# Performance work log

Hardware: AMD Instinct MI355X
Metric: run time of the kernel (lower is better)

## Reference

```python
import jax, jax.numpy as jnp
import numpy as np

THRESH = 0.5
MARGIN = 0.1
SCALE_POS = 2.0
SCALE_NEG = 50.0
EPS = 1e-5


def setup_inputs() -> dict:
    key = jax.random.key(0)
    k1, k2 = jax.random.split(key)
    B, D = 8192, 256
    feats = jax.random.normal(k1, (B, D), dtype=jnp.float32)
    # speaker embeddings are L2-normalized (cosine similarity, thresh=0.5 assumes this)
    feats = feats / jnp.linalg.norm(feats, axis=-1, keepdims=True)
    labels = jax.random.randint(k2, (B,), 0, 512, dtype=jnp.int64)
    return {"feats": feats, "labels": labels}


def reference(feats, labels):
    B = feats.shape[0]
    sim = jnp.matmul(feats, feats.T)                      # [B, B]
    same = labels[:, None] == labels[None, :]             # [B, B]

    pos_mask = same & (sim < 1.0 - EPS)                   # pos_pair_ (drops self-sim ~1)
    neg_mask = ~same                                      # neg_pair_

    neg_inf = jnp.float32(-jnp.inf)
    pos_inf = jnp.float32(jnp.inf)
    min_pos = jnp.min(jnp.where(pos_mask, sim, pos_inf), axis=1)  # min(pos_pair_)
    max_neg = jnp.max(jnp.where(neg_mask, sim, neg_inf), axis=1)  # max(neg_pair_)

    # dynamic re-masking (hard mining)
    neg_sel = neg_mask & (sim > (min_pos - MARGIN)[:, None])
    pos_sel = pos_mask & (sim < (max_neg + MARGIN)[:, None])

    valid = jnp.any(neg_sel, axis=1) & jnp.any(pos_sel, axis=1)

    # masked sums of exponentials via exp(-inf)=0; single fused mask+exp+sum
    pos_sum = jnp.sum(jnp.exp(jnp.where(pos_sel, -SCALE_POS * (sim - THRESH), neg_inf)), axis=1)
    neg_sum = jnp.sum(jnp.exp(jnp.where(neg_sel, SCALE_NEG * (sim - THRESH), neg_inf)), axis=1)

    row_loss = (1.0 / SCALE_POS) * jnp.log1p(pos_sum) + (1.0 / SCALE_NEG) * jnp.log1p(neg_sum)
    loss = jnp.sum(jnp.where(valid, row_loss, 0.0)) / B
    prec1 = jnp.mean(1.0 - valid.astype(jnp.float32))
    return loss, prec1
```

## Files before the change

kernel.cpp:

```cpp
#include <hip/hip_runtime.h>
#include <stdint.h>


typedef __attribute__((ext_vector_type(8))) short short8;
typedef __attribute__((ext_vector_type(4))) float floatx4;

constexpr int D = 256;
constexpr int BM = 128;
constexpr int NT = 64;
constexpr int NPB = NT * 8;
constexpr int BT = 512;
constexpr int CHUNK_SH = BM * 64;
constexpr int RECCAP = 2048;

__device__ __forceinline__ unsigned f2bf(float f) {
  unsigned u = __float_as_uint(f);
  return (u + 0x7FFFu + ((u >> 16) & 1u)) >> 16;
}

__device__ __forceinline__ void gl_lds16(const void* g, void* l) {
  __builtin_amdgcn_global_load_lds(
      (const __attribute__((address_space(1))) unsigned int*)g,
      (__attribute__((address_space(3))) unsigned int*)l, 16, 0, 0);
}

__device__ __forceinline__ unsigned fkey(float f) {
  unsigned b = __float_as_uint(f);
  return (b & 0x80000000u) ? ~b : (b | 0x80000000u);
}
__device__ __forceinline__ float fdec(unsigned k) {
  unsigned b = (k & 0x80000000u) ? (k & 0x7FFFFFFFu) : ~k;
  return __uint_as_float(b);
}

__device__ __forceinline__ void pair1_body(
    int bid, const unsigned short* __restrict__ fb, const int* __restrict__ labels,
    unsigned* __restrict__ kmin, unsigned* __restrict__ kmax,
    uint2* __restrict__ recs, int* __restrict__ reccnt,
    short* As, short* Bs, int* labA, int* emitCnt) {
  const int I   = bid >> 3;
  const int g   = bid & 7;
  const int nT  = (I < 32) ? 33 : 32;
  const int t0  = (g * nT) >> 3;
  const int t1  = ((g + 1) * nT) >> 3;
  const int row0 = I * BM;

  const int tid  = threadIdx.x;
  const int lane = tid & 63;
  const int wave = tid >> 6;
  const int l15  = lane & 15;
  const int quad = lane >> 4;
  const int wr   = (wave >> 1) * 32;
  const int wc   = (wave & 1) * 64;

  const float ONE_EPS = 1.0f - 1e-5f;
  const float INF = __builtin_inff();

  if (tid == 0) *emitCnt = 0;
  __syncthreads();
  if (tid < BM) labA[tid] = labels[row0 + tid];

  auto stage = [&](int b, int col0, int kc) {
#pragma unroll
    for (int j = 0; j < 2; ++j) {
      int idx = j * BT + tid;
      int r   = idx >> 3;
      int sl  = idx & 7;
      int cb  = sl ^ (r & 7);
      const char* ga = (const char*)fb + (((size_t)(row0 + r)) << 9) + (kc << 7) + (cb << 4);
      const char* gb = (const char*)fb + (((size_t)(col0 + r)) << 9) + (kc << 7) + (cb << 4);
      gl_lds16(ga, (char*)As + (size_t)b * (CHUNK_SH * 2) + ((size_t)idx << 4));
      gl_lds16(gb, (char*)Bs + (size_t)b * (CHUNK_SH * 2) + ((size_t)idx << 4));
    }
  };

  int arow[2], brow[4];
#pragma unroll
  for (int i = 0; i < 2; ++i) arow[i] = wr + i * 16 + l15;
#pragma unroll
  for (int i = 0; i < 4; ++i) brow[i] = wc + i * 16 + l15;

  float s0[8], s1[8];
#pragma unroll
  for (int i = 0; i < 8; ++i) { s0[i] = INF; s1[i] = -INF; }

  stage(0, ((I + t0) & 63) * BM, 0);

  int cur = 0;
  for (int off = t0; off < t1; ++off) {
    const int J = (I + off) & 63;
    const int col0 = J * BM;
    const bool diag = (off == 0);

    int labc[4], cidx[4];
#pragma unroll
    for (int cf = 0; cf < 4; ++cf) {
      int ci = col0 + wc + cf * 16 + l15;
      cidx[cf] = ci;
      labc[cf] = labels[ci];
    }

    floatx4 acc[2][4];
#pragma unroll
    for (int rf = 0; rf < 2; ++rf)
#pragma unroll
      for (int cf = 0; cf < 4; ++cf)
        acc[rf][cf] = (floatx4)(0.f);

#pragma unroll
    for (int kc = 0; kc < 4; ++kc) {
      if (kc < 3) {
        stage(cur ^ 1, col0, kc + 1);
        asm volatile("s_waitcnt vmcnt(4)" ::: "memory");
      } else if (off + 1 < t1) {
        stage(cur ^ 1, ((I + off + 1) & 63) * BM, 0);
        asm volatile("s_waitcnt vmcnt(4)" ::: "memory");
      } else {
        asm volatile("s_waitcnt vmcnt(0)" ::: "memory");
      }
      __builtin_amdgcn_s_barrier();
      asm volatile("" ::: "memory");

      const short* Ab = As + cur * CHUNK_SH;
      const short* Bb = Bs + cur * CHUNK_SH;
#pragma unroll
      for (int ks = 0; ks < 2; ++ks) {
        const int gg = ks * 4 + quad;
        short8 a[2], b[4];
#pragma unroll
        for (int rf = 0; rf < 2; ++rf)
          a[rf] = *(const short8*)(Ab + arow[rf] * 64 + ((gg ^ (arow[rf] & 7)) << 3));
#pragma unroll
        for (int cf = 0; cf < 4; ++cf)
          b[cf] = *(const short8*)(Bb + brow[cf] * 64 + ((gg ^ (brow[cf] & 7)) << 3));
#pragma unroll
        for (int rf = 0; rf < 2; ++rf)
#pragma unroll
          for (int cf = 0; cf < 4; ++cf)
            acc[rf][cf] = __builtin_amdgcn_mfma_f32_16x16x32_bf16(a[rf], b[cf], acc[rf][cf], 0, 0, 0);
      }
      asm volatile("s_waitcnt lgkmcnt(0)" ::: "memory");
      __builtin_amdgcn_s_barrier();
      asm volatile("" ::: "memory");
      cur ^= 1;
    }

    float c0[4], c1[4];
#pragma unroll
    for (int i = 0; i < 4; ++i) { c0[i] = INF; c1[i] = -INF; }

#pragma unroll
    for (int rf = 0; rf < 2; ++rf) {
#pragma unroll
      for (int r = 0; r < 4; ++r) {
        const int ri = wr + rf * 16 + quad * 4 + r;
        const int lr = labA[ri];
#pragma unroll
        for (int cf = 0; cf < 4; ++cf) {
          float sim = acc[rf][cf][r];
          bool same = (lr == labc[cf]);
          bool posok = same && (sim < ONE_EPS);
          float pc = posok ? sim : INF;
          float nc = same ? -INF : sim;
          s0[rf * 4 + r] = fminf(s0[rf * 4 + r], pc);
          s1[rf * 4 + r] = fmaxf(s1[rf * 4 + r], nc);
          c0[cf] = fminf(c0[cf], pc);
          c1[cf] = fmaxf(c1[cf], nc);
          bool hotn = (!same) && (sim > 0.22f);
          if (posok || hotn) {
            unsigned key = (unsigned)(row0 + ri) | ((unsigned)cidx[cf] << 13) |
                           (diag ? (1u << 26) : 0u) | (hotn ? (1u << 27) : 0u);
            int slot = atomicAdd(emitCnt, 1);
            if (slot < RECCAP)
              recs[(size_t)bid * RECCAP + slot] = make_uint2(key, __float_as_uint(sim));
          }
        }
      }
    }

    if (!diag) {
#pragma unroll
      for (int cf = 0; cf < 4; ++cf) {
        float v = c0[cf], w = c1[cf];
#pragma unroll
        for (int m = 16; m < 64; m <<= 1) {
          float vv = __shfl_xor(v, m), ww = __shfl_xor(w, m);
          v = fminf(v, vv);
          w = fmaxf(w, ww);
        }
        if (quad == 0) {
          atomicMin(&kmin[cidx[cf]], fkey(v));
          atomicMax(&kmax[cidx[cf]], fkey(w));
        }
      }
    }
  }

#pragma unroll
  for (int i = 0; i < 8; ++i) {
#pragma unroll
    for (int m = 1; m < 16; m <<= 1) {
      float v = __shfl_xor(s0[i], m), w = __shfl_xor(s1[i], m);
      s0[i] = fminf(s0[i], v);
      s1[i] = fmaxf(s1[i], w);
    }
  }
  if (l15 == 0) {
#pragma unroll
    for (int rf = 0; rf < 2; ++rf)
#pragma unroll
      for (int r = 0; r < 4; ++r) {
        int ri = row0 + wr + rf * 16 + quad * 4 + r;
        atomicMin(&kmin[ri], fkey(s0[rf * 4 + r]));
        atomicMax(&kmax[ri], fkey(s1[rf * 4 + r]));
      }
  }
  __syncthreads();
  if (tid == 0) reccnt[bid] = (*emitCnt < RECCAP) ? *emitCnt : RECCAP;
}

__device__ __forceinline__ void apply_body(
    int bid, const uint2* __restrict__ recs, const int* __restrict__ reccnt,
    const float* __restrict__ tmn, const float* __restrict__ tmx,
    float* __restrict__ pos_acc, float* __restrict__ neg_acc) {
  const int cnt = reccnt[bid];
  for (int k = threadIdx.x; k < cnt; k += blockDim.x) {
    uint2 rec = recs[(size_t)bid * RECCAP + k];
    int ri = rec.x & 8191;
    int ci = (rec.x >> 13) & 8191;
    bool dg = (rec.x >> 26) & 1;
    bool ng = (rec.x >> 27) & 1;
    float sim = __uint_as_float(rec.y);
    if (!ng) {
      float e = __expf(fmaf(-2.f, sim, 1.f));
      if (sim < tmx[ri])        atomicAdd(&pos_acc[ri], e);
      if (!dg && sim < tmx[ci]) atomicAdd(&pos_acc[ci], e);
    } else {
      float e = __expf(fmaf(50.f, sim, -25.f));
      if (sim > tmn[ri])        atomicAdd(&neg_acc[ri], e);
      if (!dg && sim > tmn[ci]) atomicAdd(&neg_acc[ci], e);
    }
  }
}

__device__ __forceinline__ void final_body(
    int T, const int* __restrict__ labels, const int* __restrict__ labcnt,
    const float* __restrict__ pos_acc, const float* __restrict__ neg_acc,
    const float* __restrict__ tmn, const float* __restrict__ tmx,
    const float* __restrict__ mpv, const float* __restrict__ mnv,
    float* __restrict__ out, float* sred) {
  const int tid = threadIdx.x;
  float loss = 0.f, cval = 0.f;
  if (tid < 128) {
    int r = T * 128 + tid;
    float a = pos_acc[r];
    float b = neg_acc[r] + (float)(8192 - labcnt[labels[r]]) * 1e-30f;
    bool valid = (mnv[r] > tmn[r]) && (mpv[r] < tmx[r]);
    if (valid) {
      loss = 0.5f * log1pf(a) + 0.02f * log1pf(b);
      cval = 1.f;
    }
  }
#pragma unroll
  for (int m = 1; m < 64; m <<= 1) {
    loss += __shfl_xor(loss, m);
    cval += __shfl_xor(cval, m);
  }
  int wv = tid >> 6, ln = tid & 63;
  if (ln == 0) { sred[wv] = loss; sred[8 + wv] = cval; }
  __syncthreads();
  if (tid == 0) {
    float L = 0.f, C = 0.f;
#pragma unroll
    for (int w = 0; w < 8; ++w) { L += sred[w]; C += sred[8 + w]; }
    atomicAdd(out, L / 8192.0f);
    atomicAdd(out + 1, -C / 8192.0f);
  }
}

__global__ void k_convert(const float* __restrict__ feats, unsigned short* __restrict__ fb,
                          float* __restrict__ pos_acc, float* __restrict__ neg_acc,
                          unsigned* __restrict__ kmin, unsigned* __restrict__ kmax,
                          int* __restrict__ labcnt, float* __restrict__ out, int n4) {
  int i = blockIdx.x * blockDim.x + threadIdx.x;
  if (i < n4) {
    float4 v = ((const float4*)feats)[i];
    unsigned lo = f2bf(v.x) | (f2bf(v.y) << 16);
    unsigned hi = f2bf(v.z) | (f2bf(v.w) << 16);
    ((uint2*)fb)[i] = make_uint2(lo, hi);
  }
  if (i < 8192) {
    pos_acc[i] = 0.f;
    neg_acc[i] = 0.f;
    kmin[i] = 0xFFFFFFFFu;
    kmax[i] = 0u;
  }
  if (i < 512) labcnt[i] = 0;
  if (i == 0) { out[0] = 0.f; out[1] = 1.f; }
}

__global__ __launch_bounds__(BT, 4)
void k_pair1(const unsigned short* __restrict__ fb, const int* __restrict__ labels,
             unsigned* __restrict__ kmin, unsigned* __restrict__ kmax,
             uint2* __restrict__ recs, int* __restrict__ reccnt) {
  __shared__ __align__(16) short As[2 * CHUNK_SH];
  __shared__ __align__(16) short Bs[2 * CHUNK_SH];
  __shared__ int labA[BM];
  __shared__ int emitCnt;
  pair1_body(blockIdx.x, fb, labels, kmin, kmax, recs, reccnt,
             As, Bs, labA, &emitCnt);
}

__global__ void k_thresh(const unsigned* __restrict__ kmin, const unsigned* __restrict__ kmax,
                         const int* __restrict__ labels, int* __restrict__ labcnt,
                         float* __restrict__ tmn, float* __restrict__ tmx,
                         float* __restrict__ mpv, float* __restrict__ mnv) {
  int r = blockIdx.x * blockDim.x + threadIdx.x;
  if (r < 8192) {
    float a = fdec(kmin[r]);
    float b = fdec(kmax[r]);
    tmn[r] = a - 0.1f;
    tmx[r] = b + 0.1f;
    mpv[r] = a;
    mnv[r] = b;
    atomicAdd(&labcnt[labels[r]], 1);
  }
}

__global__ void k_apply(const uint2* __restrict__ recs, const int* __restrict__ reccnt,
                        const float* __restrict__ tmn, const float* __restrict__ tmx,
                        float* __restrict__ pos_acc, float* __restrict__ neg_acc) {
  apply_body(blockIdx.x, recs, reccnt, tmn, tmx, pos_acc, neg_acc);
}

__global__ __launch_bounds__(BT)
void k_final(const int* __restrict__ labels, const int* __restrict__ labcnt,
             const float* __restrict__ pos_acc, const float* __restrict__ neg_acc,
             const float* __restrict__ tmn, const float* __restrict__ tmx,
             const float* __restrict__ mpv, const float* __restrict__ mnv,
             float* __restrict__ out) {
  __shared__ float sred[16];
  final_body(blockIdx.x, labels, labcnt, pos_acc, neg_acc, tmn, tmx, mpv, mnv,
             out, sred);
}

extern "C" void kernel_launch(void* const* d_in, const int* in_sizes, int n_in,
                              void* d_out, int out_size, void* d_ws, size_t ws_size,
                              hipStream_t stream) {
  const float* feats  = (const float*)d_in[0];
  const int*   labels = (const int*)d_in[1];
  const int Bn = in_sizes[1];
  float* out = (float*)d_out;

  char* base = (char*)d_ws;
  unsigned short* fb = (unsigned short*)base;
  size_t o = (size_t)Bn * D * 2;
  uint2* recs = (uint2*)(base + o); o += (size_t)NPB * RECCAP * 8;
  unsigned* kmin = (unsigned*)(base + o); o += (size_t)Bn * 4;
  unsigned* kmax = (unsigned*)(base + o); o += (size_t)Bn * 4;
  float* tmn = (float*)(base + o);  o += (size_t)Bn * 4;
  float* tmx = (float*)(base + o);  o += (size_t)Bn * 4;
  float* mpv = (float*)(base + o);  o += (size_t)Bn * 4;
  float* mnv = (float*)(base + o);  o += (size_t)Bn * 4;
  float* pos_acc = (float*)(base + o); o += (size_t)Bn * 4;
  float* neg_acc = (float*)(base + o); o += (size_t)Bn * 4;
  int* labcnt = (int*)(base + o);   o += 512 * 4;
  int* reccnt = (int*)(base + o);   o += (size_t)NPB * 4;

  int n4 = Bn * D / 4;
  k_convert<<<(n4 + 255) / 256, 256, 0, stream>>>(feats, fb, pos_acc, neg_acc,
                                                  kmin, kmax, labcnt, out, n4);
  k_pair1<<<NPB, BT, 0, stream>>>(fb, labels, kmin, kmax, recs, reccnt);
  k_thresh<<<64, 128, 0, stream>>>(kmin, kmax, labels, labcnt, tmn, tmx, mpv, mnv);
  k_apply<<<NPB, 256, 0, stream>>>(recs, reccnt, tmn, tmx, pos_acc, neg_acc);
  k_final<<<NT, BT, 0, stream>>>(labels, labcnt, pos_acc, neg_acc,
                                 tmn, tmx, mpv, mnv, out);
}
```

Measured before the change: 120.2 us.

## Keep full A row-block in LDS, stream B from global, drop thresh kernel

The pair kernel now loads the block's 128 rows × 256 bf16 A tile into LDS once and reads B fragments directly from global memory (L2) instead of double-buffering both A and B chunks through LDS with barriers. Block IDs are swizzled across XCDs so blocks sharing a row-block land on the same XCD for L2 reuse. The k_thresh kernel is removed: label counting moves into the pair kernel, and apply/final decode kmin/kmax inline. This removes a launch and the per-chunk barriers, but uncoalesced direct global B loads without prefetch may expose latency.

```diff
diff --git a/kernel.cpp b/kernel.cpp
--- a/kernel.cpp
+++ b/kernel.cpp
@@ -10,7 +10,7 @@
 constexpr int NT = 64;
 constexpr int NPB = NT * 8;
 constexpr int BT = 512;
-constexpr int CHUNK_SH = BM * 64;
+constexpr int ASH = BM * D;
 constexpr int RECCAP = 2048;
 
 __device__ __forceinline__ unsigned f2bf(float f) {
@@ -33,11 +33,16 @@
   return __uint_as_float(b);
 }
 
+__device__ __forceinline__ int xcd_swz(int b) {
+  return ((b & 7) << 6) | (b >> 3);
+}
+
 __device__ __forceinline__ void pair1_body(
     int bid, const unsigned short* __restrict__ fb, const int* __restrict__ labels,
     unsigned* __restrict__ kmin, unsigned* __restrict__ kmax,
+    int* __restrict__ labcnt,
     uint2* __restrict__ recs, int* __restrict__ reccnt,
-    short* As, short* Bs, int* labA, int* emitCnt) {
+    short* As, int* labA, int* emitCnt) {
   const int I   = bid >> 3;
   const int g   = bid & 7;
   const int nT  = (I < 32) ? 33 : 32;
@@ -58,21 +63,22 @@
 
   if (tid == 0) *emitCnt = 0;
   __syncthreads();
-  if (tid < BM) labA[tid] = labels[row0 + tid];
-
-  auto stage = [&](int b, int col0, int kc) {
-#pragma unroll
-    for (int j = 0; j < 2; ++j) {
-      int idx = j * BT + tid;
-      int r   = idx >> 3;
-      int sl  = idx & 7;
-      int cb  = sl ^ (r & 7);
-      const char* ga = (const char*)fb + (((size_t)(row0 + r)) << 9) + (kc << 7) + (cb << 4);
-      const char* gb = (const char*)fb + (((size_t)(col0 + r)) << 9) + (kc << 7) + (cb << 4);
-      gl_lds16(ga, (char*)As + (size_t)b * (CHUNK_SH * 2) + ((size_t)idx << 4));
-      gl_lds16(gb, (char*)Bs + (size_t)b * (CHUNK_SH * 2) + ((size_t)idx << 4));
-    }
-  };
+  if (tid < BM) {
+    labA[tid] = labels[row0 + tid];
+    if (g == 0) atomicAdd(&labcnt[labA[tid]], 1);
+  }
+
+#pragma unroll
+  for (int j = 0; j < 8; ++j) {
+    int idx = j * BT + tid;
+    int r   = idx >> 5;
+    int sl  = idx & 31;
+    int cb  = sl ^ (r & 7);
+    const char* ga = (const char*)fb + (((size_t)(row0 + r)) << 9) + (cb << 4);
+    gl_lds16(ga, (char*)As + ((size_t)idx << 4));
+  }
+  asm volatile("s_waitcnt vmcnt(0)" ::: "memory");
+  __syncthreads();
 
   int arow[2], brow[4];
 #pragma unroll
@@ -84,9 +90,6 @@
 #pragma unroll
   for (int i = 0; i < 8; ++i) { s0[i] = INF; s1[i] = -INF; }
 
-  stage(0, ((I + t0) & 63) * BM, 0);
-
-  int cur = 0;
   for (int off = t0; off < t1; ++off) {
     const int J = (I + off) & 63;
     const int col0 = J * BM;
@@ -108,41 +111,24 @@
         acc[rf][cf] = (floatx4)(0.f);
 
 #pragma unroll
-    for (int kc = 0; kc < 4; ++kc) {
-      if (kc < 3) {
-        stage(cur ^ 1, col0, kc + 1);
-        asm volatile("s_waitcnt vmcnt(4)" ::: "memory");
-      } else if (off + 1 < t1) {
-        stage(cur ^ 1, ((I + off + 1) & 63) * BM, 0);
-        asm volatile("s_waitcnt vmcnt(4)" ::: "memory");
-      } else {
-        asm volatile("s_waitcnt vmcnt(0)" ::: "memory");
+    for (int k = 0; k < 8; ++k) {
+      short8 b[4];
+#pragma unroll
+      for (int cf = 0; cf < 4; ++cf)
+        b[cf] = *(const short8*)((const char*)fb +
+                 (((size_t)(col0 + brow[cf])) << 9) + (k << 6) + (quad << 4));
+      short8 a[2];
+#pragma unroll
+      for (int rf = 0; rf < 2; ++rf) {
+        int row = arow[rf];
+        int ssl = ((k << 2) + quad) ^ (row & 7);
+        a[rf] = *(const short8*)(As + row * D + ssl * 8);
       }
-      __builtin_amdgcn_s_barrier();
-      asm volatile("" ::: "memory");
-
-      const short* Ab = As + cur * CHUNK_SH;
-      const short* Bb = Bs + cur * CHUNK_SH;
-#pragma unroll
-      for (int ks = 0; ks < 2; ++ks) {
-        const int gg = ks * 4 + quad;
-        short8 a[2], b[4];
-#pragma unroll
-        for (int rf = 0; rf < 2; ++rf)
-          a[rf] = *(const short8*)(Ab + arow[rf] * 64 + ((gg ^ (arow[rf] & 7)) << 3));
+#pragma unroll
+      for (int rf = 0; rf < 2; ++rf)
 #pragma unroll
         for (int cf = 0; cf < 4; ++cf)
-          b[cf] = *(const short8*)(Bb + brow[cf] * 64 + ((gg ^ (brow[cf] & 7)) << 3));
-#pragma unroll
-        for (int rf = 0; rf < 2; ++rf)
-#pragma unroll
-          for (int cf = 0; cf < 4; ++cf)
-            acc[rf][cf] = __builtin_amdgcn_mfma_f32_16x16x32_bf16(a[rf], b[cf], acc[rf][cf], 0, 0, 0);
-      }
-      asm volatile("s_waitcnt lgkmcnt(0)" ::: "memory");
-      __builtin_amdgcn_s_barrier();
-      asm volatile("" ::: "memory");
-      cur ^= 1;
+          acc[rf][cf] = __builtin_amdgcn_mfma_f32_16x16x32_bf16(a[rf], b[cf], acc[rf][cf], 0, 0, 0);
     }
 
     float c0[4], c1[4];
@@ -221,7 +207,7 @@
 
 __device__ __forceinline__ void apply_body(
     int bid, const uint2* __restrict__ recs, const int* __restrict__ reccnt,
-    const float* __restrict__ tmn, const float* __restrict__ tmx,
+    const unsigned* __restrict__ kmin, const unsigned* __restrict__ kmax,
     float* __restrict__ pos_acc, float* __restrict__ neg_acc) {
   const int cnt = reccnt[bid];
   for (int k = threadIdx.x; k < cnt; k += blockDim.x) {
@@ -233,12 +219,12 @@
     float sim = __uint_as_float(rec.y);
     if (!ng) {
       float e = __expf(fmaf(-2.f, sim, 1.f));
-      if (sim < tmx[ri])        atomicAdd(&pos_acc[ri], e);
-      if (!dg && sim < tmx[ci]) atomicAdd(&pos_acc[ci], e);
+      if (sim < fdec(kmax[ri]) + 0.1f)        atomicAdd(&pos_acc[ri], e);
+      if (!dg && sim < fdec(kmax[ci]) + 0.1f) atomicAdd(&pos_acc[ci], e);
     } else {
       float e = __expf(fmaf(50.f, sim, -25.f));
-      if (sim > tmn[ri])        atomicAdd(&neg_acc[ri], e);
-      if (!dg && sim > tmn[ci]) atomicAdd(&neg_acc[ci], e);
+      if (sim > fdec(kmin[ri]) - 0.1f)        atomicAdd(&neg_acc[ri], e);
+      if (!dg && sim > fdec(kmin[ci]) - 0.1f) atomicAdd(&neg_acc[ci], e);
     }
   }
 }
@@ -246,8 +232,7 @@
 __device__ __forceinline__ void final_body(
     int T, const int* __restrict__ labels, const int* __restrict__ labcnt,
     const float* __restrict__ pos_acc, const float* __restrict__ neg_acc,
-    const float* __restrict__ tmn, const float* __restrict__ tmx,
-    const float* __restrict__ mpv, const float* __restrict__ mnv,
+    const unsigned* __restrict__ kmin, const unsigned* __restrict__ kmax,
     float* __restrict__ out, float* sred) {
   const int tid = threadIdx.x;
   float loss = 0.f, cval = 0.f;
@@ -255,7 +240,9 @@
     int r = T * 128 + tid;
     float a = pos_acc[r];
     float b = neg_acc[r] + (float)(8192 - labcnt[labels[r]]) * 1e-30f;
-    bool valid = (mnv[r] > tmn[r]) && (mpv[r] < tmx[r]);
+    float mp = fdec(kmin[r]);
+    float mn = fdec(kmax[r]);
+    bool valid = (mn > mp - 0.1f) && (mp < mn + 0.1f);
     if (valid) {
       loss = 0.5f * log1pf(a) + 0.02f * log1pf(b);
       cval = 1.f;
@@ -302,46 +289,28 @@
 __global__ __launch_bounds__(BT, 4)
 void k_pair1(const unsigned short* __restrict__ fb, const int* __restrict__ labels,
              unsigned* __restrict__ kmin, unsigned* __restrict__ kmax,
+             int* __restrict__ labcnt,
              uint2* __restrict__ recs, int* __restrict__ reccnt) {
-  __shared__ __align__(16) short As[2 * CHUNK_SH];
-  __shared__ __align__(16) short Bs[2 * CHUNK_SH];
+  __shared__ __align__(16) short As[ASH];
   __shared__ int labA[BM];
   __shared__ int emitCnt;
-  pair1_body(blockIdx.x, fb, labels, kmin, kmax, recs, reccnt,
-             As, Bs, labA, &emitCnt);
-}
-
-__global__ void k_thresh(const unsigned* __restrict__ kmin, const unsigned* __restrict__ kmax,
-                         const int* __restrict__ labels, int* __restrict__ labcnt,
-                         float* __restrict__ tmn, float* __restrict__ tmx,
-                         float* __restrict__ mpv, float* __restrict__ mnv) {
-  int r = blockIdx.x * blockDim.x + threadIdx.x;
-  if (r < 8192) {
-    float a = fdec(kmin[r]);
-    float b = fdec(kmax[r]);
-    tmn[r] = a - 0.1f;
-    tmx[r] = b + 0.1f;
-    mpv[r] = a;
-    mnv[r] = b;
-    atomicAdd(&labcnt[labels[r]], 1);
-  }
+  pair1_body(xcd_swz((int)blockIdx.x), fb, labels, kmin, kmax, labcnt,
+             recs, reccnt, As, labA, &emitCnt);
 }
 
 __global__ void k_apply(const uint2* __restrict__ recs, const int* __restrict__ reccnt,
-                        const float* __restrict__ tmn, const float* __restrict__ tmx,
+                        const unsigned* __restrict__ kmin, const unsigned* __restrict__ kmax,
                         float* __restrict__ pos_acc, float* __restrict__ neg_acc) {
-  apply_body(blockIdx.x, recs, reccnt, tmn, tmx, pos_acc, neg_acc);
+  apply_body(blockIdx.x, recs, reccnt, kmin, kmax, pos_acc, neg_acc);
 }
 
 __global__ __launch_bounds__(BT)
 void k_final(const int* __restrict__ labels, const int* __restrict__ labcnt,
              const float* __restrict__ pos_acc, const float* __restrict__ neg_acc,
-             const float* __restrict__ tmn, const float* __restrict__ tmx,
-             const float* __restrict__ mpv, const float* __restrict__ mnv,
+             const unsigned* __restrict__ kmin, const unsigned* __restrict__ kmax,
              float* __restrict__ out) {
   __shared__ float sred[16];
-  final_body(blockIdx.x, labels, labcnt, pos_acc, neg_acc, tmn, tmx, mpv, mnv,
-             out, sred);
+  final_body(blockIdx.x, labels, labcnt, pos_acc, neg_acc, kmin, kmax, out, sred);
 }
 
 extern "C" void kernel_launch(void* const* d_in, const int* in_sizes, int n_in,
@@ -358,10 +327,6 @@
   uint2* recs = (uint2*)(base + o); o += (size_t)NPB * RECCAP * 8;
   unsigned* kmin = (unsigned*)(base + o); o += (size_t)Bn * 4;
   unsigned* kmax = (unsigned*)(base + o); o += (size_t)Bn * 4;
-  float* tmn = (float*)(base + o);  o += (size_t)Bn * 4;
-  float* tmx = (float*)(base + o);  o += (size_t)Bn * 4;
-  float* mpv = (float*)(base + o);  o += (size_t)Bn * 4;
-  float* mnv = (float*)(base + o);  o += (size_t)Bn * 4;
   float* pos_acc = (float*)(base + o); o += (size_t)Bn * 4;
   float* neg_acc = (float*)(base + o); o += (size_t)Bn * 4;
   int* labcnt = (int*)(base + o);   o += 512 * 4;
@@ -370,9 +335,8 @@
   int n4 = Bn * D / 4;
   k_convert<<<(n4 + 255) / 256, 256, 0, stream>>>(feats, fb, pos_acc, neg_acc,
                                                   kmin, kmax, labcnt, out, n4);
-  k_pair1<<<NPB, BT, 0, stream>>>(fb, labels, kmin, kmax, recs, reccnt);
-  k_thresh<<<64, 128, 0, stream>>>(kmin, kmax, labels, labcnt, tmn, tmx, mpv, mnv);
-  k_apply<<<NPB, 256, 0, stream>>>(recs, reccnt, tmn, tmx, pos_acc, neg_acc);
+  k_pair1<<<NPB, BT, 0, stream>>>(fb, labels, kmin, kmax, labcnt, recs, reccnt);
+  k_apply<<<NPB, 256, 0, stream>>>(recs, reccnt, kmin, kmax, pos_acc, neg_acc);
   k_final<<<NT, BT, 0, stream>>>(labels, labcnt, pos_acc, neg_acc,
-                                 tmn, tmx, mpv, mnv, out);
-}
+                                 kmin, kmax, out);
+}
```

Result: slower. 163.0 us (+35.6%).
